# Kernel tuning notes

Hardware: AMD Instinct MI355X
Metric: run time of the kernel (lower is better)

The kernel has to match this reference:

```python
import jax, jax.numpy as jnp
import numpy as np

N_NODES = 50000
N_EDGES = 800000
C = 128


def setup_inputs() -> dict:
    key = jax.random.key(0)
    ks = jax.random.split(key, 7)
    X_real = jax.random.normal(ks[0], (N_NODES, C), dtype=jnp.float32)
    X_imag = jax.random.normal(ks[1], (N_NODES, C), dtype=jnp.float32)
    # sparse normalized Laplacian values (real/imag parts), COO format
    L_real_vals = jax.random.normal(ks[2], (N_EDGES,), dtype=jnp.float32) * 0.1
    L_imag_vals = jax.random.normal(ks[3], (N_EDGES,), dtype=jnp.float32) * 0.1
    weight = jax.random.normal(ks[4], (C, C), dtype=jnp.float32) * (1.0 / np.sqrt(C))
    row = jax.random.randint(ks[5], (N_EDGES,), 0, N_NODES, dtype=jnp.int32)
    col = jax.random.randint(ks[6], (N_EDGES,), 0, N_NODES, dtype=jnp.int32)
    return {"X_real": X_real, "X_imag": X_imag,
            "L_real_vals": L_real_vals, "L_imag_vals": L_imag_vals,
            "weight": weight, "row": row, "col": col}


def reference(X_real, X_imag, L_real_vals, L_imag_vals, weight, row, col):
    n = X_real.shape[0]

    def spmm(vals, X):
        # sparse [N,N] @ dense [N,C] via gather + segment-sum scatter
        return jax.ops.segment_sum(vals[:, None] * X[col], row, num_segments=n)

    # complex Laplacian application: (Lr + i Li)(Xr + i Xi)
    # real = Lr@Xr - Li@Xi ; imag = Li@Xr + Lr@Xi ; then shared dense projection W
    agg_real = spmm(L_real_vals, X_real) - spmm(L_imag_vals, X_imag)  # [N, C]
    agg_imag = spmm(L_imag_vals, X_real) + spmm(L_real_vals, X_imag)  # [N, C]
    result_real = agg_real @ weight
    result_imag = agg_imag @ weight
    # residual add as in forward()
    return (result_real + X_real, result_imag + X_imag)
```

## Files before the change

### kernel.cpp

```cpp
#include <hip/hip_runtime.h>
#include <cstddef>

#define CC 128

typedef __attribute__((ext_vector_type(8))) short bf16x8;
typedef __attribute__((ext_vector_type(4))) float f32x4;


__global__ __launch_bounds__(256) void hist_rank(
    const int* __restrict__ row, int* __restrict__ counts,
    int* __restrict__ rank, int N, int E)
{
    const int base = (blockIdx.x * 256 + threadIdx.x) * 4;
    if (base + 3 < E) {
        const int4 r4 = *(const int4*)(row + base);
        int4 k4;
        k4.x = atomicAdd(counts + 0 * N + r4.x, 1);
        k4.y = atomicAdd(counts + 1 * N + r4.y, 1);
        k4.z = atomicAdd(counts + 2 * N + r4.z, 1);
        k4.w = atomicAdd(counts + 3 * N + r4.w, 1);
        *(int4*)(rank + base) = k4;
    } else {
        for (int e = base; e < E; ++e)
            rank[e] = atomicAdd(counts + (size_t)(e & 3) * N + row[e], 1);
    }
}

__global__ __launch_bounds__(256) void scan_block_reduce(
    const int* __restrict__ counts, int* __restrict__ bsum, int N)
{
    __shared__ int s[256];
    const int t = threadIdx.x;
    const int idx = blockIdx.x * 256 + t;
    int v = 0;
    if (idx < N)
        v = counts[idx] + counts[N + idx] + counts[2 * N + idx]
          + counts[3 * N + idx];
    s[t] = v;
    __syncthreads();
    #pragma unroll
    for (int off = 128; off > 0; off >>= 1) {
        if (t < off) s[t] += s[t + off];
        __syncthreads();
    }
    if (t == 0) bsum[blockIdx.x] = s[0];
}

__global__ __launch_bounds__(256) void scan_bsum(
    const int* __restrict__ bsum, int* __restrict__ bpre, int NB)
{
    __shared__ int s[256];
    const int t = threadIdx.x;
    s[t] = (t < NB) ? bsum[t] : 0;
    __syncthreads();
    #pragma unroll
    for (int off = 1; off < 256; off <<= 1) {
        const int v = s[t];
        const int u = (t >= off) ? s[t - off] : 0;
        __syncthreads();
        s[t] = v + u;
        __syncthreads();
    }
    if (t < NB) bpre[t] = t ? s[t - 1] : 0;
}

__global__ __launch_bounds__(256) void scan_final(
    const int* __restrict__ counts, const int* __restrict__ bpre,
    int* __restrict__ rbase, int N)
{
    __shared__ int s[256];
    const int t = threadIdx.x;
    const int idx = blockIdx.x * 256 + t;
    int c0 = 0, c1 = 0, c2 = 0, c3 = 0;
    if (idx < N) {
        c0 = counts[idx];
        c1 = counts[N + idx];
        c2 = counts[2 * N + idx];
        c3 = counts[3 * N + idx];
    }
    const int v = c0 + c1 + c2 + c3;
    s[t] = v;
    __syncthreads();
    #pragma unroll
    for (int off = 1; off < 256; off <<= 1) {
        const int a = s[t];
        const int u = (t >= off) ? s[t - off] : 0;
        __syncthreads();
        s[t] = a + u;
        __syncthreads();
    }
    if (idx < N) {
        const int off = bpre[blockIdx.x] + s[t] - v;
        rbase[idx]         = off;
        rbase[N + idx]     = off + c0;
        rbase[2 * N + idx] = off + c0 + c1;
        rbase[3 * N + idx] = off + c0 + c1 + c2;
    }
}

__global__ __launch_bounds__(256) void fill_csr_rank(
    const int* __restrict__ row, const int* __restrict__ col,
    const float* __restrict__ Lr, const float* __restrict__ Li,
    const int* __restrict__ rbase, const int* __restrict__ rank,
    int4* __restrict__ meta, int N, int E)
{
    const int base = (blockIdx.x * 256 + threadIdx.x) * 4;
    if (base + 3 < E) {
        const int4   r4 = *(const int4*)(row + base);
        const int4   c4 = *(const int4*)(col + base);
        const float4 a4 = *(const float4*)(Lr + base);
        const float4 b4 = *(const float4*)(Li + base);
        const int4   k4 = *(const int4*)(rank + base);
        meta[rbase[r4.x] + k4.x] =
            make_int4(c4.x, __float_as_int(a4.x), __float_as_int(b4.x), 0);
        meta[rbase[N + r4.y] + k4.y] =
            make_int4(c4.y, __float_as_int(a4.y), __float_as_int(b4.y), 0);
        meta[rbase[2 * N + r4.z] + k4.z] =
            make_int4(c4.z, __float_as_int(a4.z), __float_as_int(b4.z), 0);
        meta[rbase[3 * N + r4.w] + k4.w] =
            make_int4(c4.w, __float_as_int(a4.w), __float_as_int(b4.w), 0);
    } else {
        for (int e = base; e < E; ++e)
            meta[rbase[(size_t)(e & 3) * N + row[e]] + rank[e]] =
                make_int4(col[e], __float_as_int(Lr[e]), __float_as_int(Li[e]), 0);
    }
}

__device__ __forceinline__ unsigned short f2bf(float f)
{
    unsigned int u = __float_as_uint(f);
    u = (u + 0x7fffu + ((u >> 16) & 1u)) >> 16;
    return (unsigned short)u;
}

__device__ __forceinline__ unsigned int pack2(float a, float b)
{
    return (unsigned int)f2bf(a) | ((unsigned int)f2bf(b) << 16);
}

__global__ __launch_bounds__(256) void conv_w(
    const float* __restrict__ W, unsigned short* __restrict__ Wt)
{
    const int idx = blockIdx.x * 256 + threadIdx.x;
    if (idx >= CC * CC) return;
    const int k = idx >> 7;
    const int n = idx & 127;
    const unsigned int sw = ((unsigned)(2 * k) ^ (((unsigned)n & 7u) << 4)) >> 1;
    Wt[(size_t)n * 128 + sw] = f2bf(W[idx]);
}

__global__ __launch_bounds__(256) void gemm_xw_mfma(
    const float* __restrict__ Xr, const float* __restrict__ Xi,
    const unsigned short* __restrict__ Wt,
    unsigned short* __restrict__ Y, int N)
{
    __shared__ unsigned short Bs[128 * 128];
    __shared__ unsigned short As[64 * 128];
    const int t = threadIdx.x;
    const int m0 = blockIdx.x * 64;
    const int M = 2 * N;

    {
        const uint4* src = (const uint4*)Wt;
        uint4* dst = (uint4*)Bs;
        #pragma unroll
        for (int i = 0; i < 8; ++i) dst[t + 256 * i] = src[t + 256 * i];
    }
    #pragma unroll
    for (int i = 0; i < 4; ++i) {
        const int blk = t + 256 * i;
        const int r  = blk >> 4;
        const int k0 = (blk & 15) * 8;
        const int m  = m0 + r;
        float4 q0 = make_float4(0.f, 0.f, 0.f, 0.f);
        float4 q1 = make_float4(0.f, 0.f, 0.f, 0.f);
        if (m < M) {
            const float* src = (m < N) ? (Xr + (size_t)m * CC)
                                       : (Xi + (size_t)(m - N) * CC);
            q0 = *(const float4*)(src + k0);
            q1 = *(const float4*)(src + k0 + 4);
        }
        uint4 h;
        h.x = pack2(q0.x, q0.y);
        h.y = pack2(q0.z, q0.w);
        h.z = pack2(q1.x, q1.y);
        h.w = pack2(q1.z, q1.w);
        const int byte = r * 256 + ((2 * k0) ^ ((r & 7) << 4));
        *(uint4*)((char*)As + byte) = h;
    }
    __syncthreads();

    const int w = t >> 6, lane = t & 63;
    const int wr = w >> 1, wc = w & 1;
    const int r0 = wr * 32;
    const int c0 = wc * 64;
    const int lr = lane & 15;
    const int lk = lane >> 4;

    f32x4 acc[2][4];
    #pragma unroll
    for (int a = 0; a < 2; ++a)
        #pragma unroll
        for (int b = 0; b < 4; ++b)
            acc[a][b] = (f32x4){0.f, 0.f, 0.f, 0.f};

    #pragma unroll
    for (int kk = 0; kk < 4; ++kk) {
        const int kbase = kk * 32 + lk * 8;
        bf16x8 afrag[2];
        #pragma unroll
        for (int at = 0; at < 2; ++at) {
            const int row = r0 + at * 16 + lr;
            afrag[at] = *(const bf16x8*)((const char*)As +
                row * 256 + ((2 * kbase) ^ ((row & 7) << 4)));
        }
        #pragma unroll
        for (int bt = 0; bt < 4; ++bt) {
            const int col = c0 + bt * 16 + lr;
            const bf16x8 bfrag = *(const bf16x8*)((const char*)Bs +
                col * 256 + ((2 * kbase) ^ ((col & 7) << 4)));
            acc[0][bt] = __builtin_amdgcn_mfma_f32_16x16x32_bf16(
                afrag[0], bfrag, acc[0][bt], 0, 0, 0);
            acc[1][bt] = __builtin_amdgcn_mfma_f32_16x16x32_bf16(
                afrag[1], bfrag, acc[1][bt], 0, 0, 0);
        }
    }

    #pragma unroll
    for (int at = 0; at < 2; ++at) {
        #pragma unroll
        for (int v = 0; v < 4; ++v) {
            const int m = m0 + r0 + at * 16 + lk * 4 + v;
            if (m >= M) continue;
            const int node = (m < N) ? m : m - N;
            const int half = (m < N) ? 0 : 128;
            unsigned short* dst = Y + (size_t)node * 256 + half;
            #pragma unroll
            for (int bt = 0; bt < 4; ++bt)
                dst[c0 + bt * 16 + lr] = f2bf(acc[at][bt][v]);
        }
    }
}

__device__ __forceinline__ void cmadd_bf(
    const int4 m, const unsigned int ur, const unsigned int ui,
    float2& aR, float2& aI)
{
    const float lr = __int_as_float(m.y);
    const float li = __int_as_float(m.z);
    const float yrx = __uint_as_float(ur << 16);
    const float yry = __uint_as_float(ur & 0xFFFF0000u);
    const float yix = __uint_as_float(ui << 16);
    const float yiy = __uint_as_float(ui & 0xFFFF0000u);
    aR.x += lr * yrx - li * yix;
    aR.y += lr * yry - li * yiy;
    aI.x += li * yrx + lr * yix;
    aI.y += li * yry + lr * yiy;
}

__device__ __forceinline__ void edge_acc(
    const int4 m, const unsigned short* __restrict__ Y,
    int lane, float2& aR, float2& aI)
{
    const unsigned short* b = Y + (size_t)m.x * 256 + 2 * lane;
    const unsigned int ur = *(const unsigned int*)(b);
    const unsigned int ui = *(const unsigned int*)(b + 128);
    cmadd_bf(m, ur, ui, aR, aI);
}

__global__ __launch_bounds__(256) void gather_fused(
    const unsigned short* __restrict__ Y,
    const float* __restrict__ Xr, const float* __restrict__ Xi,
    const int* __restrict__ offsets, const int4* __restrict__ meta,
    float* __restrict__ out, int N, int E)
{
    const int n = blockIdx.x * 4 + (threadIdx.x >> 6);
    if (n >= N) return;
    const int lane = threadIdx.x & 63;
    const int start = offsets[n];
    const int end   = (n + 1 < N) ? offsets[n + 1] : E;
    const int Em1 = E - 1;

    float2 aR = *(const float2*)(Xr + (size_t)n * CC + 2 * lane);
    float2 aI = *(const float2*)(Xi + (size_t)n * CC + 2 * lane);

    int4 m0 = meta[min(start + 0, Em1)];
    int4 m1 = meta[min(start + 1, Em1)];
    int4 m2 = meta[min(start + 2, Em1)];
    int4 m3 = meta[min(start + 3, Em1)];
    int4 m4 = meta[min(start + 4, Em1)];
    int4 m5 = meta[min(start + 5, Em1)];
    int4 m6 = meta[min(start + 6, Em1)];
    int4 m7 = meta[min(start + 7, Em1)];

    int j = start;
    for (; j + 8 <= end; j += 8) {
        const int4 n0 = meta[min(j +  8, Em1)];
        const int4 n1 = meta[min(j +  9, Em1)];
        const int4 n2 = meta[min(j + 10, Em1)];
        const int4 n3 = meta[min(j + 11, Em1)];
        const int4 n4 = meta[min(j + 12, Em1)];
        const int4 n5 = meta[min(j + 13, Em1)];
        const int4 n6 = meta[min(j + 14, Em1)];
        const int4 n7 = meta[min(j + 15, Em1)];
        const unsigned short* b0 = Y + (size_t)m0.x * 256 + 2 * lane;
        const unsigned short* b1 = Y + (size_t)m1.x * 256 + 2 * lane;
        const unsigned short* b2 = Y + (size_t)m2.x * 256 + 2 * lane;
        const unsigned short* b3 = Y + (size_t)m3.x * 256 + 2 * lane;
        const unsigned short* b4 = Y + (size_t)m4.x * 256 + 2 * lane;
        const unsigned short* b5 = Y + (size_t)m5.x * 256 + 2 * lane;
        const unsigned short* b6 = Y + (size_t)m6.x * 256 + 2 * lane;
        const unsigned short* b7 = Y + (size_t)m7.x * 256 + 2 * lane;
        const unsigned int ur0 = *(const unsigned int*)(b0);
        const unsigned int ui0 = *(const unsigned int*)(b0 + 128);
        const unsigned int ur1 = *(const unsigned int*)(b1);
        const unsigned int ui1 = *(const unsigned int*)(b1 + 128);
        const unsigned int ur2 = *(const unsigned int*)(b2);
        const unsigned int ui2 = *(const unsigned int*)(b2 + 128);
        const unsigned int ur3 = *(const unsigned int*)(b3);
        const unsigned int ui3 = *(const unsigned int*)(b3 + 128);
        const unsigned int ur4 = *(const unsigned int*)(b4);
        const unsigned int ui4 = *(const unsigned int*)(b4 + 128);
        const unsigned int ur5 = *(const unsigned int*)(b5);
        const unsigned int ui5 = *(const unsigned int*)(b5 + 128);
        const unsigned int ur6 = *(const unsigned int*)(b6);
        const unsigned int ui6 = *(const unsigned int*)(b6 + 128);
        const unsigned int ur7 = *(const unsigned int*)(b7);
        const unsigned int ui7 = *(const unsigned int*)(b7 + 128);

        cmadd_bf(m0, ur0, ui0, aR, aI);
        cmadd_bf(m1, ur1, ui1, aR, aI);
        cmadd_bf(m2, ur2, ui2, aR, aI);
        cmadd_bf(m3, ur3, ui3, aR, aI);
        cmadd_bf(m4, ur4, ui4, aR, aI);
        cmadd_bf(m5, ur5, ui5, aR, aI);
        cmadd_bf(m6, ur6, ui6, aR, aI);
        cmadd_bf(m7, ur7, ui7, aR, aI);

        m0 = n0; m1 = n1; m2 = n2; m3 = n3;
        m4 = n4; m5 = n5; m6 = n6; m7 = n7;
    }
    const int r = end - j;
    if (r > 0) edge_acc(m0, Y, lane, aR, aI);
    if (r > 1) edge_acc(m1, Y, lane, aR, aI);
    if (r > 2) edge_acc(m2, Y, lane, aR, aI);
    if (r > 3) edge_acc(m3, Y, lane, aR, aI);
    if (r > 4) edge_acc(m4, Y, lane, aR, aI);
    if (r > 5) edge_acc(m5, Y, lane, aR, aI);
    if (r > 6) edge_acc(m6, Y, lane, aR, aI);

    *(float2*)(out + (size_t)n * CC + 2 * lane) = aR;
    *(float2*)(out + ((size_t)n + N) * CC + 2 * lane) = aI;
}

__global__ __launch_bounds__(256) void gather_nodes(
    const float* __restrict__ Xr, const float* __restrict__ Xi,
    const int* __restrict__ offsets, const int4* __restrict__ meta,
    float* __restrict__ out, int N, int E)
{
    const int n = blockIdx.x * 4 + (threadIdx.x >> 6);
    if (n >= N) return;
    const int lane = threadIdx.x & 63;
    const int start = offsets[n];
    const int end   = (n + 1 < N) ? offsets[n + 1] : E;
    float2 aR = make_float2(0.f, 0.f);
    float2 aI = make_float2(0.f, 0.f);
    for (int j = start; j < end; ++j) {
        const int4 m0 = meta[j];
        const float2 xr0 = *(const float2*)(Xr + (size_t)m0.x * CC + 2 * lane);
        const float2 xi0 = *(const float2*)(Xi + (size_t)m0.x * CC + 2 * lane);
        const float lr0 = __int_as_float(m0.y), li0 = __int_as_float(m0.z);
        aR.x += lr0 * xr0.x - li0 * xi0.x;
        aR.y += lr0 * xr0.y - li0 * xi0.y;
        aI.x += li0 * xr0.x + lr0 * xi0.x;
        aI.y += li0 * xr0.y + lr0 * xi0.y;
    }
    *(float2*)(out + (size_t)n * CC + 2 * lane) = aR;
    *(float2*)(out + ((size_t)n + N) * CC + 2 * lane) = aI;
}

__global__ __launch_bounds__(256) void scatter_edges(
    const float* __restrict__ Xr, const float* __restrict__ Xi,
    const float* __restrict__ Lr, const float* __restrict__ Li,
    const int* __restrict__ row, const int* __restrict__ col,
    float* __restrict__ out, int N, int E)
{
    const int e = blockIdx.x * 4 + (threadIdx.x >> 6);
    if (e >= E) return;
    const int lane = threadIdx.x & 63;
    const int r = row[e], c = col[e];
    const float lr = Lr[e];
    const float li = Li[e];
    const float2 xr = *(const float2*)(Xr + (size_t)c * CC + 2 * lane);
    const float2 xi = *(const float2*)(Xi + (size_t)c * CC + 2 * lane);
    float* pr = out + (size_t)r * CC + 2 * lane;
    float* pi = out + ((size_t)r + N) * CC + 2 * lane;
    unsafeAtomicAdd(pr,     lr * xr.x - li * xi.x);
    unsafeAtomicAdd(pr + 1, lr * xr.y - li * xi.y);
    unsafeAtomicAdd(pi,     li * xr.x + lr * xi.x);
    unsafeAtomicAdd(pi + 1, li * xr.y + lr * xi.y);
}

__global__ __launch_bounds__(256) void gemm_inplace(
    float* __restrict__ io, const float* __restrict__ W,
    const float* __restrict__ Xp, int N)
{
    __shared__ float Ws[64 * CC];
    __shared__ float AsT[CC][36];
    const int t = threadIdx.x;
    const int m0 = blockIdx.x * 32;

    for (int ch = t; ch < 1024; ch += 256) {
        const int r  = ch >> 5;
        const int k0 = (ch & 31) * 4;
        const int m  = m0 + r;
        float4 q = make_float4(0.f, 0.f, 0.f, 0.f);
        if (m < N) q = *(const float4*)(io + (size_t)m * CC + k0);
        AsT[k0 + 0][r] = q.x;
        AsT[k0 + 1][r] = q.y;
        AsT[k0 + 2][r] = q.z;
        AsT[k0 + 3][r] = q.w;
    }

    const int cg = t & 31;
    const int rs = t >> 5;
    float s[4][4];
    #pragma unroll
    for (int a = 0; a < 4; ++a)
        #pragma unroll
        for (int b = 0; b < 4; ++b) s[a][b] = 0.f;

    for (int kc = 0; kc < 2; ++kc) {
        __syncthreads();
        {
            const float4* src = (const float4*)(W + (size_t)kc * 64 * CC);
            float4* dst = (float4*)Ws;
            #pragma unroll
            for (int i = 0; i < 8; ++i) dst[t + 256 * i] = src[t + 256 * i];
        }
        __syncthreads();
        #pragma unroll 4
        for (int kk = 0; kk < 64; ++kk) {
            const int k = kc * 64 + kk;
            const float4 av = *(const float4*)&AsT[k][rs * 4];
            const float4 wv = *(const float4*)&Ws[kk * CC + cg * 4];
            const float ar[4] = {av.x, av.y, av.z, av.w};
            const float wc[4] = {wv.x, wv.y, wv.z, wv.w};
            #pragma unroll
            for (int a = 0; a < 4; ++a)
                #pragma unroll
                for (int b = 0; b < 4; ++b) s[a][b] += ar[a] * wc[b];
        }
    }

    #pragma unroll
    for (int a = 0; a < 4; ++a) {
        const int m = m0 + rs * 4 + a;
        if (m >= N) continue;
        const float4 xv = *(const float4*)(Xp + (size_t)m * CC + cg * 4);
        float4 o;
        o.x = s[a][0] + xv.x;
        o.y = s[a][1] + xv.y;
        o.z = s[a][2] + xv.z;
        o.w = s[a][3] + xv.w;
        *(float4*)(io + (size_t)m * CC + cg * 4) = o;
    }
}

extern "C" void kernel_launch(void* const* d_in, const int* in_sizes, int n_in,
                              void* d_out, int out_size, void* d_ws, size_t ws_size,
                              hipStream_t stream)
{
    const float* Xr = (const float*)d_in[0];
    const float* Xi = (const float*)d_in[1];
    const float* Lr = (const float*)d_in[2];
    const float* Li = (const float*)d_in[3];
    const float* W  = (const float*)d_in[4];
    const int* row = (const int*)d_in[5];
    const int* col = (const int*)d_in[6];
    float* out = (float*)d_out;

    const int N = in_sizes[0] / CC;
    const int E = in_sizes[2];
    const int NB = (N + 255) / 256;
    const int EB4 = ((E + 3) / 4 + 255) / 256;

    const size_t y_bytes    = (size_t)N * 256 * sizeof(unsigned short);
    const size_t wt_bytes   = (size_t)CC * CC * sizeof(unsigned short);
    const size_t meta_bytes = (size_t)E * 16;
    const size_t int_bytes  = ((size_t)8 * N + 512 + E) * sizeof(int);
    const size_t need_csr   = meta_bytes + int_bytes;
    const size_t need_fused = y_bytes + wt_bytes + need_csr;

    if (ws_size >= need_fused) {
        unsigned short* Y  = (unsigned short*)d_ws;
        unsigned short* Wt = (unsigned short*)((char*)d_ws + y_bytes);
        int4*  meta   = (int4*)((char*)d_ws + y_bytes + wt_bytes);
        int*   counts = (int*)((char*)d_ws + y_bytes + wt_bytes + meta_bytes);
        int*   rbase  = counts + 4 * N;
        int*   bsum   = rbase + 4 * N;
        int*   bpre   = bsum + 256;
        int*   rank   = bpre + 256;

        hipMemsetAsync(counts, 0, (size_t)4 * N * sizeof(int), stream);
        hist_rank<<<dim3(EB4), dim3(256), 0, stream>>>(row, counts, rank, N, E);
        scan_block_reduce<<<dim3(NB), dim3(256), 0, stream>>>(counts, bsum, N);
        scan_bsum<<<dim3(1), dim3(256), 0, stream>>>(bsum, bpre, NB);
        scan_final<<<dim3(NB), dim3(256), 0, stream>>>(counts, bpre, rbase, N);
        fill_csr_rank<<<dim3(EB4), dim3(256), 0, stream>>>(
            row, col, Lr, Li, rbase, rank, meta, N, E);
        conv_w<<<dim3((CC * CC + 255) / 256), dim3(256), 0, stream>>>(W, Wt);
        gemm_xw_mfma<<<dim3((2 * N + 63) / 64), dim3(256), 0, stream>>>(
            Xr, Xi, Wt, Y, N);
        gather_fused<<<dim3((N + 3) / 4), dim3(256), 0, stream>>>(
            Y, Xr, Xi, rbase , meta, out, N, E);
    } else if (ws_size >= need_csr) {
        int4* meta    = (int4*)d_ws;
        int*  counts  = (int*)((char*)d_ws + meta_bytes);
        int*  rbase   = counts + 4 * N;
        int*  bsum    = rbase + 4 * N;
        int*  bpre    = bsum + 256;
        int*  rank    = bpre + 256;

        hipMemsetAsync(counts, 0, (size_t)4 * N * sizeof(int), stream);
        hist_rank<<<dim3(EB4), dim3(256), 0, stream>>>(row, counts, rank, N, E);
        scan_block_reduce<<<dim3(NB), dim3(256), 0, stream>>>(counts, bsum, N);
        scan_bsum<<<dim3(1), dim3(256), 0, stream>>>(bsum, bpre, NB);
        scan_final<<<dim3(NB), dim3(256), 0, stream>>>(counts, bpre, rbase, N);
        fill_csr_rank<<<dim3(EB4), dim3(256), 0, stream>>>(
            row, col, Lr, Li, rbase, rank, meta, N, E);
        gather_nodes<<<dim3((N + 3) / 4), dim3(256), 0, stream>>>(
            Xr, Xi, rbase, meta, out, N, E);
        gemm_inplace<<<dim3((N + 31) / 32), dim3(256), 0, stream>>>(out, W, Xr, N);
        gemm_inplace<<<dim3((N + 31) / 32), dim3(256), 0, stream>>>(
            out + (size_t)N * CC, W, Xi, N);
    } else {
        hipMemsetAsync(out, 0, (size_t)2 * N * CC * sizeof(float), stream);
        scatter_edges<<<dim3((E + 3) / 4), dim3(256), 0, stream>>>(
            Xr, Xi, Lr, Li, row, col, out, N, E);
        gemm_inplace<<<dim3((N + 31) / 32), dim3(256), 0, stream>>>(out, W, Xr, N);
        gemm_inplace<<<dim3((N + 31) / 32), dim3(256), 0, stream>>>(
            out + (size_t)N * CC, W, Xi, N);
    }
}
```

Baseline: 251.5 us.

## Fuse XW GEMM with row histogram in one interleaved launch, drop conv_w

Merges the bf16 MFMA GEMM and the atomic row histogram into a single launch whose blocks are interleaved between the two roles, so the compute-bound GEMM overlaps with the atomic-bound histogram. It also removes the separate weight-conversion kernel: each GEMM block now converts W to swizzled bf16 straight into shared memory. This cuts two launches, but every GEMM block repeats the 64KB W read and conversion, and the fused kernel uses 48KB of static shared memory even in the histogram blocks, which may limit occupancy.

```diff
diff --git a/kernel.cpp b/kernel.cpp
--- a/kernel.cpp
+++ b/kernel.cpp
@@ -6,12 +6,23 @@
 typedef __attribute__((ext_vector_type(8))) short bf16x8;
 typedef __attribute__((ext_vector_type(4))) float f32x4;
 
-
-__global__ __launch_bounds__(256) void hist_rank(
+__device__ __forceinline__ unsigned short f2bf(float f)
+{
+    unsigned int u = __float_as_uint(f);
+    u = (u + 0x7fffu + ((u >> 16) & 1u)) >> 16;
+    return (unsigned short)u;
+}
+
+__device__ __forceinline__ unsigned int pack2(float a, float b)
+{
+    return (unsigned int)f2bf(a) | ((unsigned int)f2bf(b) << 16);
+}
+
+
+__device__ __forceinline__ void hist_quad(
     const int* __restrict__ row, int* __restrict__ counts,
-    int* __restrict__ rank, int N, int E)
-{
-    const int base = (blockIdx.x * 256 + threadIdx.x) * 4;
+    int* __restrict__ rank, int N, int E, int base)
+{
     if (base + 3 < E) {
         const int4 r4 = *(const int4*)(row + base);
         int4 k4;
@@ -26,146 +37,34 @@
     }
 }
 
-__global__ __launch_bounds__(256) void scan_block_reduce(
-    const int* __restrict__ counts, int* __restrict__ bsum, int N)
-{
-    __shared__ int s[256];
-    const int t = threadIdx.x;
-    const int idx = blockIdx.x * 256 + t;
-    int v = 0;
-    if (idx < N)
-        v = counts[idx] + counts[N + idx] + counts[2 * N + idx]
-          + counts[3 * N + idx];
-    s[t] = v;
-    __syncthreads();
-    #pragma unroll
-    for (int off = 128; off > 0; off >>= 1) {
-        if (t < off) s[t] += s[t + off];
-        __syncthreads();
-    }
-    if (t == 0) bsum[blockIdx.x] = s[0];
-}
-
-__global__ __launch_bounds__(256) void scan_bsum(
-    const int* __restrict__ bsum, int* __restrict__ bpre, int NB)
-{
-    __shared__ int s[256];
-    const int t = threadIdx.x;
-    s[t] = (t < NB) ? bsum[t] : 0;
-    __syncthreads();
-    #pragma unroll
-    for (int off = 1; off < 256; off <<= 1) {
-        const int v = s[t];
-        const int u = (t >= off) ? s[t - off] : 0;
-        __syncthreads();
-        s[t] = v + u;
-        __syncthreads();
-    }
-    if (t < NB) bpre[t] = t ? s[t - 1] : 0;
-}
-
-__global__ __launch_bounds__(256) void scan_final(
-    const int* __restrict__ counts, const int* __restrict__ bpre,
-    int* __restrict__ rbase, int N)
-{
-    __shared__ int s[256];
-    const int t = threadIdx.x;
-    const int idx = blockIdx.x * 256 + t;
-    int c0 = 0, c1 = 0, c2 = 0, c3 = 0;
-    if (idx < N) {
-        c0 = counts[idx];
-        c1 = counts[N + idx];
-        c2 = counts[2 * N + idx];
-        c3 = counts[3 * N + idx];
-    }
-    const int v = c0 + c1 + c2 + c3;
-    s[t] = v;
-    __syncthreads();
-    #pragma unroll
-    for (int off = 1; off < 256; off <<= 1) {
-        const int a = s[t];
-        const int u = (t >= off) ? s[t - off] : 0;
-        __syncthreads();
-        s[t] = a + u;
-        __syncthreads();
-    }
-    if (idx < N) {
-        const int off = bpre[blockIdx.x] + s[t] - v;
-        rbase[idx]         = off;
-        rbase[N + idx]     = off + c0;
-        rbase[2 * N + idx] = off + c0 + c1;
-        rbase[3 * N + idx] = off + c0 + c1 + c2;
-    }
-}
-
-__global__ __launch_bounds__(256) void fill_csr_rank(
-    const int* __restrict__ row, const int* __restrict__ col,
-    const float* __restrict__ Lr, const float* __restrict__ Li,
-    const int* __restrict__ rbase, const int* __restrict__ rank,
-    int4* __restrict__ meta, int N, int E)
-{
-    const int base = (blockIdx.x * 256 + threadIdx.x) * 4;
-    if (base + 3 < E) {
-        const int4   r4 = *(const int4*)(row + base);
-        const int4   c4 = *(const int4*)(col + base);
-        const float4 a4 = *(const float4*)(Lr + base);
-        const float4 b4 = *(const float4*)(Li + base);
-        const int4   k4 = *(const int4*)(rank + base);
-        meta[rbase[r4.x] + k4.x] =
-            make_int4(c4.x, __float_as_int(a4.x), __float_as_int(b4.x), 0);
-        meta[rbase[N + r4.y] + k4.y] =
-            make_int4(c4.y, __float_as_int(a4.y), __float_as_int(b4.y), 0);
-        meta[rbase[2 * N + r4.z] + k4.z] =
-            make_int4(c4.z, __float_as_int(a4.z), __float_as_int(b4.z), 0);
-        meta[rbase[3 * N + r4.w] + k4.w] =
-            make_int4(c4.w, __float_as_int(a4.w), __float_as_int(b4.w), 0);
-    } else {
-        for (int e = base; e < E; ++e)
-            meta[rbase[(size_t)(e & 3) * N + row[e]] + rank[e]] =
-                make_int4(col[e], __float_as_int(Lr[e]), __float_as_int(Li[e]), 0);
-    }
-}
-
-__device__ __forceinline__ unsigned short f2bf(float f)
-{
-    unsigned int u = __float_as_uint(f);
-    u = (u + 0x7fffu + ((u >> 16) & 1u)) >> 16;
-    return (unsigned short)u;
-}
-
-__device__ __forceinline__ unsigned int pack2(float a, float b)
-{
-    return (unsigned int)f2bf(a) | ((unsigned int)f2bf(b) << 16);
-}
-
-__global__ __launch_bounds__(256) void conv_w(
-    const float* __restrict__ W, unsigned short* __restrict__ Wt)
-{
-    const int idx = blockIdx.x * 256 + threadIdx.x;
-    if (idx >= CC * CC) return;
-    const int k = idx >> 7;
-    const int n = idx & 127;
-    const unsigned int sw = ((unsigned)(2 * k) ^ (((unsigned)n & 7u) << 4)) >> 1;
-    Wt[(size_t)n * 128 + sw] = f2bf(W[idx]);
-}
-
-__global__ __launch_bounds__(256) void gemm_xw_mfma(
+__device__ __forceinline__ void gemm_stage_B_from_W(
+    const float* __restrict__ W, unsigned short* Bs, int t)
+{
+    #pragma unroll
+    for (int i = 0; i < 16; ++i) {
+        const int idx4 = (t + 256 * i) * 4;
+        const int k  = idx4 >> 7;
+        const int n0 = idx4 & 127;
+        const float4 w4 = *(const float4*)(W + idx4);
+        *(unsigned short*)((char*)Bs + (n0 + 0) * 256 +
+            ((2 * k) ^ (((n0 + 0) & 7) << 4))) = f2bf(w4.x);
+        *(unsigned short*)((char*)Bs + (n0 + 1) * 256 +
+            ((2 * k) ^ (((n0 + 1) & 7) << 4))) = f2bf(w4.y);
+        *(unsigned short*)((char*)Bs + (n0 + 2) * 256 +
+            ((2 * k) ^ (((n0 + 2) & 7) << 4))) = f2bf(w4.z);
+        *(unsigned short*)((char*)Bs + (n0 + 3) * 256 +
+            ((2 * k) ^ (((n0 + 3) & 7) << 4))) = f2bf(w4.w);
+    }
+}
+
+__device__ __forceinline__ void gemm_tile(
     const float* __restrict__ Xr, const float* __restrict__ Xi,
-    const unsigned short* __restrict__ Wt,
-    unsigned short* __restrict__ Y, int N)
-{
-    __shared__ unsigned short Bs[128 * 128];
-    __shared__ unsigned short As[64 * 128];
-    const int t = threadIdx.x;
-    const int m0 = blockIdx.x * 64;
+    unsigned short* __restrict__ Y, int N, int bid,
+    const unsigned short* Bs, unsigned short* As, int t)
+{
+    const int m0 = bid * 64;
     const int M = 2 * N;
 
-    {
-        const uint4* src = (const uint4*)Wt;
-        uint4* dst = (uint4*)Bs;
-        #pragma unroll
-        for (int i = 0; i < 8; ++i) dst[t + 256 * i] = src[t + 256 * i];
-    }
     #pragma unroll
     for (int i = 0; i < 4; ++i) {
         const int blk = t + 256 * i;
@@ -240,6 +139,136 @@
                 dst[c0 + bt * 16 + lr] = f2bf(acc[at][bt][v]);
         }
     }
+}
+
+__global__ __launch_bounds__(256) void gemm_hist_fused(
+    const float* __restrict__ Xr, const float* __restrict__ Xi,
+    const float* __restrict__ W, unsigned short* __restrict__ Y,
+    const int* __restrict__ row, int* __restrict__ counts,
+    int* __restrict__ rank, int N, int E, int G_gemm, int total)
+{
+    __shared__ char smem[49152];
+    const int bid = blockIdx.x;
+    const long long pg  = (long long)bid * G_gemm / total;
+    const long long pg1 = (long long)(bid + 1) * G_gemm / total;
+    if (pg1 > pg) {
+        unsigned short* Bs = (unsigned short*)smem;
+        unsigned short* As = (unsigned short*)(smem + 32768);
+        gemm_stage_B_from_W(W, Bs, threadIdx.x);
+        gemm_tile(Xr, Xi, Y, N, (int)pg, Bs, As, threadIdx.x);
+    } else {
+        const int hb = bid - (int)pg;
+        hist_quad(row, counts, rank, N, E, (hb * 256 + threadIdx.x) * 4);
+    }
+}
+
+__global__ __launch_bounds__(256) void scan_block_reduce(
+    const int* __restrict__ counts, int* __restrict__ bsum, int N)
+{
+    __shared__ int s[256];
+    const int t = threadIdx.x;
+    const int idx = blockIdx.x * 256 + t;
+    int v = 0;
+    if (idx < N)
+        v = counts[idx] + counts[N + idx] + counts[2 * N + idx]
+          + counts[3 * N + idx];
+    s[t] = v;
+    __syncthreads();
+    #pragma unroll
+    for (int off = 128; off > 0; off >>= 1) {
+        if (t < off) s[t] += s[t + off];
+        __syncthreads();
+    }
+    if (t == 0) bsum[blockIdx.x] = s[0];
+}
+
+__global__ __launch_bounds__(256) void scan_bsum(
+    const int* __restrict__ bsum, int* __restrict__ bpre, int NB)
+{
+    __shared__ int s[256];
+    const int t = threadIdx.x;
+    s[t] = (t < NB) ? bsum[t] : 0;
+    __syncthreads();
+    #pragma unroll
+    for (int off = 1; off < 256; off <<= 1) {
+        const int v = s[t];
+        const int u = (t >= off) ? s[t - off] : 0;
+        __syncthreads();
+        s[t] = v + u;
+        __syncthreads();
+    }
+    if (t < NB) bpre[t] = t ? s[t - 1] : 0;
+}
+
+__global__ __launch_bounds__(256) void scan_final(
+    const int* __restrict__ counts, const int* __restrict__ bpre,
+    int* __restrict__ rbase, int N)
+{
+    __shared__ int s[256];
+    const int t = threadIdx.x;
+    const int idx = blockIdx.x * 256 + t;
+    int c0 = 0, c1 = 0, c2 = 0, c3 = 0;
+    if (idx < N) {
+        c0 = counts[idx];
+        c1 = counts[N + idx];
+        c2 = counts[2 * N + idx];
+        c3 = counts[3 * N + idx];
+    }
+    const int v = c0 + c1 + c2 + c3;
+    s[t] = v;
+    __syncthreads();
+    #pragma unroll
+    for (int off = 1; off < 256; off <<= 1) {
+        const int a = s[t];
+        const int u = (t >= off) ? s[t - off] : 0;
+        __syncthreads();
+        s[t] = a + u;
+        __syncthreads();
+    }
+    if (idx < N) {
+        const int off = bpre[blockIdx.x] + s[t] - v;
+        rbase[idx]         = off;
+        rbase[N + idx]     = off + c0;
+        rbase[2 * N + idx] = off + c0 + c1;
+        rbase[3 * N + idx] = off + c0 + c1 + c2;
+    }
+}
+
+__device__ __forceinline__ void fill_quad(
+    const int* __restrict__ row, const int* __restrict__ col,
+    const float* __restrict__ Lr, const float* __restrict__ Li,
+    const int* __restrict__ rbase, const int* __restrict__ rank,
+    int4* __restrict__ meta, int N, int E, int base)
+{
+    if (base + 3 < E) {
+        const int4   r4 = *(const int4*)(row + base);
+        const int4   c4 = *(const int4*)(col + base);
+        const float4 a4 = *(const float4*)(Lr + base);
+        const float4 b4 = *(const float4*)(Li + base);
+        const int4   k4 = *(const int4*)(rank + base);
+        meta[rbase[r4.x] + k4.x] =
+            make_int4(c4.x, __float_as_int(a4.x), __float_as_int(b4.x), 0);
+        meta[rbase[N + r4.y] + k4.y] =
+            make_int4(c4.y, __float_as_int(a4.y), __float_as_int(b4.y), 0);
+        meta[rbase[2 * N + r4.z] + k4.z] =
+            make_int4(c4.z, __float_as_int(a4.z), __float_as_int(b4.z), 0);
+        meta[rbase[3 * N + r4.w] + k4.w] =
+            make_int4(c4.w, __float_as_int(a4.w), __float_as_int(b4.w), 0);
+    } else {
+        for (int e = base; e < E; ++e)
+            meta[rbase[(size_t)(e & 3) * N + row[e]] + rank[e]] =
+                make_int4(col[e], __float_as_int(Lr[e]), __float_as_int(Li[e]), 0);
+    }
+}
+
+__global__ __launch_bounds__(256) void fill_csr_rank(
+    const int* __restrict__ row, const int* __restrict__ col,
+    const float* __restrict__ Lr, const float* __restrict__ Li,
+    const int* __restrict__ rbase, const int* __restrict__ rank,
+    int4* __restrict__ meta, int N, int E)
+{
+    fill_quad(row, col, Lr, Li, rbase, rank, meta, N, E,
+              (blockIdx.x * 256 + threadIdx.x) * 4);
 }
 
 __device__ __forceinline__ void cmadd_bf(
@@ -353,6 +382,14 @@
     *(float2*)(out + ((size_t)n + N) * CC + 2 * lane) = aI;
 }
 
+__global__ __launch_bounds__(256) void hist_rank_fb(
+    const int* __restrict__ row, int* __restrict__ counts,
+    int* __restrict__ rank, int N, int E)
+{
+    hist_quad(row, counts, rank, N, E,
+              (blockIdx.x * 256 + threadIdx.x) * 4);
+}
+
 __global__ __launch_bounds__(256) void gather_nodes(
     const float* __restrict__ Xr, const float* __restrict__ Xi,
     const int* __restrict__ offsets, const int4* __restrict__ meta,
@@ -422,7 +459,7 @@
         AsT[k0 + 3][r] = q.w;
     }
 
-    const int cg = t & 31;
+    const int cg_ = t & 31;
     const int rs = t >> 5;
     float s[4][4];
     #pragma unroll
@@ -443,7 +480,7 @@
         for (int kk = 0; kk < 64; ++kk) {
             const int k = kc * 64 + kk;
             const float4 av = *(const float4*)&AsT[k][rs * 4];
-            const float4 wv = *(const float4*)&Ws[kk * CC + cg * 4];
+            const float4 wv = *(const float4*)&Ws[kk * CC + cg_ * 4];
             const float ar[4] = {av.x, av.y, av.z, av.w};
             const float wc[4] = {wv.x, wv.y, wv.z, wv.w};
             #pragma unroll
@@ -457,13 +494,13 @@
     for (int a = 0; a < 4; ++a) {
         const int m = m0 + rs * 4 + a;
         if (m >= N) continue;
-        const float4 xv = *(const float4*)(Xp + (size_t)m * CC + cg * 4);
+        const float4 xv = *(const float4*)(Xp + (size_t)m * CC + cg_ * 4);
         float4 o;
         o.x = s[a][0] + xv.x;
         o.y = s[a][1] + xv.y;
         o.z = s[a][2] + xv.z;
         o.w = s[a][3] + xv.w;
-        *(float4*)(io + (size_t)m * CC + cg * 4) = o;
+        *(float4*)(io + (size_t)m * CC + cg_ * 4) = o;
     }
 }
 
@@ -484,34 +521,32 @@
     const int E = in_sizes[2];
     const int NB = (N + 255) / 256;
     const int EB4 = ((E + 3) / 4 + 255) / 256;
+    const int G_gemm = (2 * N + 63) / 64;
+    const int G_total = G_gemm + EB4;
 
     const size_t y_bytes    = (size_t)N * 256 * sizeof(unsigned short);
-    const size_t wt_bytes   = (size_t)CC * CC * sizeof(unsigned short);
     const size_t meta_bytes = (size_t)E * 16;
     const size_t int_bytes  = ((size_t)8 * N + 512 + E) * sizeof(int);
     const size_t need_csr   = meta_bytes + int_bytes;
-    const size_t need_fused = y_bytes + wt_bytes + need_csr;
+    const size_t need_fused = y_bytes + need_csr;
 
     if (ws_size >= need_fused) {
-        unsigned short* Y  = (unsigned short*)d_ws;
-        unsigned short* Wt = (unsigned short*)((char*)d_ws + y_bytes);
-        int4*  meta   = (int4*)((char*)d_ws + y_bytes + wt_bytes);
-        int*   counts = (int*)((char*)d_ws + y_bytes + wt_bytes + meta_bytes);
+        unsigned short* Y = (unsigned short*)d_ws;
+        int4*  meta   = (int4*)((char*)d_ws + y_bytes);
+        int*   counts = (int*)((char*)d_ws + y_bytes + meta_bytes);
         int*   rbase  = counts + 4 * N;
         int*   bsum   = rbase + 4 * N;
         int*   bpre   = bsum + 256;
         int*   rank   = bpre + 256;
 
         hipMemsetAsync(counts, 0, (size_t)4 * N * sizeof(int), stream);
-        hist_rank<<<dim3(EB4), dim3(256), 0, stream>>>(row, counts, rank, N, E);
+        gemm_hist_fused<<<dim3(G_total), dim3(256), 0, stream>>>(
+            Xr, Xi, W, Y, row, counts, rank, N, E, G_gemm, G_total);
         scan_block_reduce<<<dim3(NB), dim3(256), 0, stream>>>(counts, bsum, N);
         scan_bsum<<<dim3(1), dim3(256), 0, stream>>>(bsum, bpre, NB);
         scan_final<<<dim3(NB), dim3(256), 0, stream>>>(counts, bpre, rbase, N);
         fill_csr_rank<<<dim3(EB4), dim3(256), 0, stream>>>(
             row, col, Lr, Li, rbase, rank, meta, N, E);
-        conv_w<<<dim3((CC * CC + 255) / 256), dim3(256), 0, stream>>>(W, Wt);
-        gemm_xw_mfma<<<dim3((2 * N + 63) / 64), dim3(256), 0, stream>>>(
-            Xr, Xi, Wt, Y, N);
         gather_fused<<<dim3((N + 3) / 4), dim3(256), 0, stream>>>(
             Y, Xr, Xi, rbase , meta, out, N, E);
     } else if (ws_size >= need_csr) {
@@ -523,7 +558,7 @@
         int*  rank    = bpre + 256;
 
         hipMemsetAsync(counts, 0, (size_t)4 * N * sizeof(int), stream);
-        hist_rank<<<dim3(EB4), dim3(256), 0, stream>>>(row, counts, rank, N, E);
+        hist_rank_fb<<<dim3(EB4), dim3(256), 0, stream>>>(row, counts, rank, N, E);
         scan_block_reduce<<<dim3(NB), dim3(256), 0, stream>>>(counts, bsum, N);
         scan_bsum<<<dim3(1), dim3(256), 0, stream>>>(bsum, bpre, NB);
         scan_final<<<dim3(NB), dim3(256), 0, stream>>>(counts, bpre, rbase, N);
```

After: 249.9 us. No clear change (-0.6%).
